# Optimization experiments

Hardware: AMD Instinct MI355X
Metric: run time of the kernel (lower is better)

The kernel has to match this reference:

```python
import jax, jax.numpy as jnp
import numpy as np

MD = 4  # max displacement -> 9x9 = 81 window, matches the +8 pad and 81 output channels


def setup_inputs() -> dict:
    key = jax.random.key(0)
    k1, k2 = jax.random.split(key)
    first = jax.random.normal(k1, (8, 256, 96, 128), dtype=jnp.float32)
    second = jax.random.normal(k2, (8, 256, 96, 128), dtype=jnp.float32)
    return {"first": first, "second": second}


def reference(first, second):
    # first, second: [B, C, H, W]
    B, C, H, W = first.shape
    # pad second spatially by MD on each side (the rbot1 [B, H+8, W+8, C] buffer)
    pad = jnp.pad(second, ((0, 0), (0, 0), (MD, MD), (MD, MD)))
    outs = []
    # channel ordering matches CUDA kernel: top_channel = (dy+4)*9 + (dx+4)
    for dy in range(2 * MD + 1):
        for dx in range(2 * MD + 1):
            shifted = jax.lax.dynamic_slice(pad, (0, 0, dy, dx), (B, C, H, W))
            outs.append(jnp.einsum('bchw,bchw->bhw', first, shifted))
    # kernel divides the per-pixel dot product by the channel count
    return jnp.stack(outs, axis=1) / C  # [B, 81, H, W]
```

## Files before the change

### kernel.cpp

```cpp
#include <hip/hip_runtime.h>

namespace {
constexpr int Bn = 8, Cn = 256, Hn = 96, Wn = 128;
constexpr int HWn = Hn * Wn;
constexpr int CHWn = Cn * HWn;
constexpr int ND = 9;
constexpr int TILESH = Hn / 4;
constexpr int NBLK = Bn * TILESH * ND;
constexpr int PERX = NBLK / 8;
}

__device__ __forceinline__ float dpp_shr1(float x) {
  return __int_as_float(__builtin_amdgcn_update_dpp(
      0, __float_as_int(x), 0x111 , 0xF, 0xF, true));
}
__device__ __forceinline__ float dpp_shl1(float x) {
  return __int_as_float(__builtin_amdgcn_update_dpp(
      0, __float_as_int(x), 0x101 , 0xF, 0xF, true));
}

struct Ch {
  float4 sa, sb, fa, fb;
};

__global__ __launch_bounds__(64, 2) void corr_kernel(
    const float* __restrict__ first, const float* __restrict__ second,
    float* __restrict__ out)
{
  const int lane = threadIdx.x;
  const int bid = blockIdx.x;
  const int logical = (bid & 7) * PERX + (bid >> 3);
  const int dy = logical % ND;
  const int t = logical / ND;
  const int b = t / TILESH;
  const int h0 = (t % TILESH) * 4;

  const int hs = lane >> 4;
  const int w0 = (lane & 15) << 3;

  const int gr = h0 + hs + dy - 4;
  const float m = (gr >= 0 && gr < Hn) ? 1.0f : 0.0f;
  const int cg = min(max(gr, 0), Hn - 1);

  const float* ssrc = second + b * CHWn + cg * Wn + w0;
  const float* fsrc = first + b * CHWn + (h0 + hs) * Wn + w0;

  float acc[ND][8];
#pragma unroll
  for (int dx = 0; dx < ND; ++dx)
#pragma unroll
    for (int p = 0; p < 8; ++p) acc[dx][p] = 0.f;

  auto LOADCH = [&](int coff) -> Ch {
    Ch r;
    r.sa = *(const float4*)(ssrc + coff);
    r.sb = *(const float4*)(ssrc + coff + 4);
    r.fa = *(const float4*)(fsrc + coff);
    r.fb = *(const float4*)(fsrc + coff + 4);
    return r;
  };

  auto COMP = [&](const Ch& ch) {
    const float sa0 = ch.sa.x * m, sa1 = ch.sa.y * m, sa2 = ch.sa.z * m, sa3 = ch.sa.w * m;
    const float sb0 = ch.sb.x * m, sb1 = ch.sb.y * m, sb2 = ch.sb.z * m, sb3 = ch.sb.w * m;
    const float s[16] = {
        dpp_shr1(sb0), dpp_shr1(sb1), dpp_shr1(sb2), dpp_shr1(sb3),
        sa0, sa1, sa2, sa3,
        sb0, sb1, sb2, sb3,
        dpp_shl1(sa0), dpp_shl1(sa1), dpp_shl1(sa2), dpp_shl1(sa3)};
    const float f[8] = {ch.fa.x, ch.fa.y, ch.fa.z, ch.fa.w,
                        ch.fb.x, ch.fb.y, ch.fb.z, ch.fb.w};
#pragma unroll
    for (int dx = 0; dx < ND; ++dx)
#pragma unroll
      for (int p = 0; p < 8; ++p)
        acc[dx][p] = fmaf(f[p], s[p + dx], acc[dx][p]);
  };

  Ch L0 = LOADCH(0);
  Ch L1 = LOADCH(HWn);
  int coff = 2 * HWn;
#pragma unroll 1
  for (int it = 0; it < (Cn - 2) / 2; ++it) {
    Ch N0 = LOADCH(coff);
    Ch N1 = LOADCH(coff + HWn);
    COMP(L0);
    COMP(L1);
    L0 = N0;
    L1 = N1;
    coff += 2 * HWn;
  }
  COMP(L0);
  COMP(L1);

  const float sc = 1.0f / Cn;
  float* obase = out + ((b * 81 + dy * ND) * Hn + (h0 + hs)) * Wn + w0;
#pragma unroll
  for (int dx = 0; dx < ND; ++dx) {
    float4 o0 = make_float4(acc[dx][0] * sc, acc[dx][1] * sc,
                            acc[dx][2] * sc, acc[dx][3] * sc);
    float4 o1 = make_float4(acc[dx][4] * sc, acc[dx][5] * sc,
                            acc[dx][6] * sc, acc[dx][7] * sc);
    *(float4*)(obase + dx * HWn) = o0;
    *(float4*)(obase + dx * HWn + 4) = o1;
  }
}

extern "C" void kernel_launch(void* const* d_in, const int* in_sizes, int n_in,
                              void* d_out, int out_size, void* d_ws, size_t ws_size,
                              hipStream_t stream) {
  const float* first = (const float*)d_in[0];
  const float* second = (const float*)d_in[1];
  float* out = (float*)d_out;
  corr_kernel<<<dim3(NBLK), dim3(64), 0, stream>>>(first, second, out);
}
```

Measured before the change: 98.27 us.

## Rewrite correlation as bf16 MFMA banded matmul with LDS double buffering

Replaces the scalar FP32 FMA correlation kernel with a block-tiled kernel. Each block stages first and padded second tiles in LDS as bf16, double-buffered across channel chunks of 32. It computes 32x32 banded dot-product tiles with MFMA 32x32x16 bf16 instructions, keeping only the 9-wide diagonal band per dy. Results are transposed through LDS so output stores are coalesced. This trades FP32 accuracy for bf16 inputs and wastes MFMA work on off-band entries, aiming to cut the FMA-bound compute cost.

```diff
diff --git a/kernel.cpp b/kernel.cpp
--- a/kernel.cpp
+++ b/kernel.cpp
@@ -1,108 +1,188 @@
 #include <hip/hip_runtime.h>
+
+typedef __attribute__((ext_vector_type(8))) short bf16x8;
+typedef __attribute__((ext_vector_type(16))) float f32x16;
 
 namespace {
 constexpr int Bn = 8, Cn = 256, Hn = 96, Wn = 128;
 constexpr int HWn = Hn * Wn;
-constexpr int CHWn = Cn * HWn;
-constexpr int ND = 9;
-constexpr int TILESH = Hn / 4;
-constexpr int NBLK = Bn * TILESH * ND;
-constexpr int PERX = NBLK / 8;
+constexpr int KC = 32;
+constexpr int SP = 40;
+constexpr int SW = 72;
+constexpr int SR = 6;
+constexpr int FW = 64;
+constexpr int SSZ = SR * SW * SP;
+constexpr int FSZ = (4 * FW + 8) * SP;
+constexpr int BUF = SSZ + FSZ;
+constexpr int NBLK = 8 * 24 * 2 * 3;
 }
 
-__device__ __forceinline__ float dpp_shr1(float x) {
-  return __int_as_float(__builtin_amdgcn_update_dpp(
-      0, __float_as_int(x), 0x111 , 0xF, 0xF, true));
-}
-__device__ __forceinline__ float dpp_shl1(float x) {
-  return __int_as_float(__builtin_amdgcn_update_dpp(
-      0, __float_as_int(x), 0x101 , 0xF, 0xF, true));
+__device__ __forceinline__ unsigned f2bfpk(float lo, float hi) {
+  unsigned a = __float_as_uint(lo), b = __float_as_uint(hi);
+  a = ((a + 0x7FFF + ((a >> 16) & 1)) >> 16) & 0xFFFF;
+  b = ((b + 0x7FFF + ((b >> 16) & 1)) >> 16) & 0xFFFF;
+  return (b << 16) | a;
 }
 
-struct Ch {
-  float4 sa, sb, fa, fb;
-};
-
-__global__ __launch_bounds__(64, 2) void corr_kernel(
+__global__ __launch_bounds__(768, 1) void corr_mfma(
     const float* __restrict__ first, const float* __restrict__ second,
     float* __restrict__ out)
 {
-  const int lane = threadIdx.x;
+  __shared__ __align__(16) unsigned short LB[2][BUF];
+
+  const int tid = threadIdx.x;
+  const int wv = tid >> 6;
+  const int lane = tid & 63;
+  const int ln31 = lane & 31;
+  const int half = lane >> 5;
+  const int li4 = lane >> 2;
+  const int lm4 = lane & 3;
+
   const int bid = blockIdx.x;
-  const int logical = (bid & 7) * PERX + (bid >> 3);
-  const int dy = logical % ND;
-  const int t = logical / ND;
-  const int b = t / TILESH;
-  const int h0 = (t % TILESH) * 4;
+  const int logical = (bid & 7) * (NBLK / 8) + (bid >> 3);
+  const int b = logical / 144;
+  int rest = logical % 144;
+  const int hq = rest / 6; rest %= 6;
+  const int wh = rest / 3;
+  const int dg = rest % 3;
+  const int h0 = hq * 4, wb = wh * 64;
+  const int rbase = h0 + dg * 3 - 4;
 
-  const int hs = lane >> 4;
-  const int w0 = (lane & 15) << 3;
+  const int hh = wv / 3;
+  const int tt = wv % 3;
+  const int toff = (tt == 0) ? 0 : (tt == 1) ? 24 : 40;
 
-  const int gr = h0 + hs + dy - 4;
-  const float m = (gr >= 0 && gr < Hn) ? 1.0f : 0.0f;
-  const int cg = min(max(gr, 0), Hn - 1);
+  f32x16 acc0 = {}, acc1 = {}, acc2 = {};
 
-  const float* ssrc = second + b * CHWn + cg * Wn + w0;
-  const float* fsrc = first + b * CHWn + (h0 + hs) * Wn + w0;
+  float sx[16][2];
 
-  float acc[ND][8];
+  auto LOADS = [&](int ck) {
 #pragma unroll
-  for (int dx = 0; dx < ND; ++dx)
+    for (int st = 0; st < 8; ++st) {
+      const int id = wv * 8 + st;
+      const int r = id >> 4, q = id & 15;
+      const int cl = ((q >> 2) << 3) + (lm4 << 1);
+      const int wi = ((q & 3) << 4) + li4;
+      const int rg = rbase + r, wg = wb - 4 + wi;
+      const int rgc = min(Hn - 1, max(0, rg));
+      const int wgc = min(Wn - 1, max(0, wg));
+      const bool v = (rg >= 0) & (rg < Hn) & (wg >= 0) & (wg < Wn);
+      const float* p = second + ((b * Cn + ck + cl) * Hn + rgc) * Wn + wgc;
+      sx[st][0] = v ? p[0] : 0.0f;
+      sx[st][1] = v ? p[HWn] : 0.0f;
+    }
 #pragma unroll
-    for (int p = 0; p < 8; ++p) acc[dx][p] = 0.f;
-
-  auto LOADCH = [&](int coff) -> Ch {
-    Ch r;
-    r.sa = *(const float4*)(ssrc + coff);
-    r.sb = *(const float4*)(ssrc + coff + 4);
-    r.fa = *(const float4*)(fsrc + coff);
-    r.fb = *(const float4*)(fsrc + coff + 4);
-    return r;
+    for (int pt = 0; pt < 2; ++pt) {
+      const int id = wv * 2 + pt;
+      const int r = id >> 2, cbi = id & 3;
+      const int cl = (cbi << 3) + (lm4 << 1);
+      const int wi = 64 + li4;
+      const int rg = rbase + r, wg = wb - 4 + wi;
+      const int rgc = min(Hn - 1, max(0, rg));
+      const int wgc = min(Wn - 1, max(0, wg));
+      const bool v = (lane < 32) & (rg >= 0) & (rg < Hn) & (wg >= 0) & (wg < Wn);
+      const float* p = second + ((b * Cn + ck + cl) * Hn + rgc) * Wn + wgc;
+      sx[8 + pt][0] = v ? p[0] : 0.0f;
+      sx[8 + pt][1] = v ? p[HWn] : 0.0f;
+    }
+#pragma unroll
+    for (int k = 0; k < 6; ++k) {
+      const int ft = wv + 12 * k;
+      if (ft < 64) {
+        const int hh2 = ft >> 4, q = ft & 15;
+        const int cl = ((q >> 2) << 3) + (lm4 << 1);
+        const int wl = ((q & 3) << 4) + li4;
+        const float* p = first + ((b * Cn + ck + cl) * Hn + h0 + hh2) * Wn + wb + wl;
+        sx[10 + k][0] = p[0];
+        sx[10 + k][1] = p[HWn];
+      }
+    }
   };
 
-  auto COMP = [&](const Ch& ch) {
-    const float sa0 = ch.sa.x * m, sa1 = ch.sa.y * m, sa2 = ch.sa.z * m, sa3 = ch.sa.w * m;
-    const float sb0 = ch.sb.x * m, sb1 = ch.sb.y * m, sb2 = ch.sb.z * m, sb3 = ch.sb.w * m;
-    const float s[16] = {
-        dpp_shr1(sb0), dpp_shr1(sb1), dpp_shr1(sb2), dpp_shr1(sb3),
-        sa0, sa1, sa2, sa3,
-        sb0, sb1, sb2, sb3,
-        dpp_shl1(sa0), dpp_shl1(sa1), dpp_shl1(sa2), dpp_shl1(sa3)};
-    const float f[8] = {ch.fa.x, ch.fa.y, ch.fa.z, ch.fa.w,
-                        ch.fb.x, ch.fb.y, ch.fb.z, ch.fb.w};
+  auto WRITES = [&](unsigned short* lb) {
 #pragma unroll
-    for (int dx = 0; dx < ND; ++dx)
+    for (int st = 0; st < 8; ++st) {
+      const int id = wv * 8 + st;
+      const int r = id >> 4, q = id & 15;
+      const int cl = ((q >> 2) << 3) + (lm4 << 1);
+      const int wi = ((q & 3) << 4) + li4;
+      *(unsigned*)&lb[(r * SW + wi) * SP + cl] = f2bfpk(sx[st][0], sx[st][1]);
+    }
 #pragma unroll
-      for (int p = 0; p < 8; ++p)
-        acc[dx][p] = fmaf(f[p], s[p + dx], acc[dx][p]);
+    for (int pt = 0; pt < 2; ++pt) {
+      const int id = wv * 2 + pt;
+      const int r = id >> 2, cbi = id & 3;
+      const int cl = (cbi << 3) + (lm4 << 1);
+      const int wi = 64 + li4;
+      if (lane < 32)
+        *(unsigned*)&lb[(r * SW + wi) * SP + cl] = f2bfpk(sx[8 + pt][0], sx[8 + pt][1]);
+    }
+#pragma unroll
+    for (int k = 0; k < 6; ++k) {
+      const int ft = wv + 12 * k;
+      if (ft < 64) {
+        const int hh2 = ft >> 4, q = ft & 15;
+        const int cl = ((q >> 2) << 3) + (lm4 << 1);
+        const int wl = ((q & 3) << 4) + li4;
+        *(unsigned*)&lb[SSZ + (hh2 * FW + wl) * SP + cl] = f2bfpk(sx[10 + k][0], sx[10 + k][1]);
+      }
+    }
   };
 
-  Ch L0 = LOADCH(0);
-  Ch L1 = LOADCH(HWn);
-  int coff = 2 * HWn;
-#pragma unroll 1
-  for (int it = 0; it < (Cn - 2) / 2; ++it) {
-    Ch N0 = LOADCH(coff);
-    Ch N1 = LOADCH(coff + HWn);
-    COMP(L0);
-    COMP(L1);
-    L0 = N0;
-    L1 = N1;
-    coff += 2 * HWn;
+  auto COMPUTE = [&](const unsigned short* sb) {
+    const unsigned short* fb = sb + SSZ;
+    const int abase = (hh * FW + toff + ln31) * SP + (half << 3);
+    bf16x8 a0 = *(const bf16x8*)(fb + abase);
+    bf16x8 a1 = *(const bf16x8*)(fb + abase + 16);
+    const int b0 = ((hh + 0) * SW + toff + ln31) * SP + (half << 3);
+    const int b1 = b0 + SW * SP;
+    const int b2 = b1 + SW * SP;
+    bf16x8 s00 = *(const bf16x8*)(sb + b0);
+    bf16x8 s01 = *(const bf16x8*)(sb + b0 + 16);
+    bf16x8 s10 = *(const bf16x8*)(sb + b1);
+    bf16x8 s11 = *(const bf16x8*)(sb + b1 + 16);
+    bf16x8 s20 = *(const bf16x8*)(sb + b2);
+    bf16x8 s21 = *(const bf16x8*)(sb + b2 + 16);
+    acc0 = __builtin_amdgcn_mfma_f32_32x32x16_bf16(a0, s00, acc0, 0, 0, 0);
+    acc0 = __builtin_amdgcn_mfma_f32_32x32x16_bf16(a1, s01, acc0, 0, 0, 0);
+    acc1 = __builtin_amdgcn_mfma_f32_32x32x16_bf16(a0, s10, acc1, 0, 0, 0);
+    acc1 = __builtin_amdgcn_mfma_f32_32x32x16_bf16(a1, s11, acc1, 0, 0, 0);
+    acc2 = __builtin_amdgcn_mfma_f32_32x32x16_bf16(a0, s20, acc2, 0, 0, 0);
+    acc2 = __builtin_amdgcn_mfma_f32_32x32x16_bf16(a1, s21, acc2, 0, 0, 0);
+  };
+
+  LOADS(0);
+  WRITES(&LB[0][0]);
+  __syncthreads();
+
+#pragma unroll 2
+  for (int k = 0; k < 8; ++k) {
+    if (k < 7) LOADS((k + 1) * KC);
+    COMPUTE(&LB[k & 1][0]);
+    if (k < 7) WRITES(&LB[(k + 1) & 1][0]);
+    __syncthreads();
   }
-  COMP(L0);
-  COMP(L1);
 
-  const float sc = 1.0f / Cn;
-  float* obase = out + ((b * 81 + dy * ND) * Hn + (h0 + hs)) * Wn + w0;
+  float* outl = (float*)&LB[0][0];
+  const float sc = 1.0f / 256.0f;
 #pragma unroll
-  for (int dx = 0; dx < ND; ++dx) {
-    float4 o0 = make_float4(acc[dx][0] * sc, acc[dx][1] * sc,
-                            acc[dx][2] * sc, acc[dx][3] * sc);
-    float4 o1 = make_float4(acc[dx][4] * sc, acc[dx][5] * sc,
-                            acc[dx][6] * sc, acc[dx][7] * sc);
-    *(float4*)(obase + dx * HWn) = o0;
-    *(float4*)(obase + dx * HWn + 4) = o1;
+  for (int dd = 0; dd < 3; ++dd) {
+    const f32x16& A = (dd == 0) ? acc0 : (dd == 1) ? acc1 : acc2;
+#pragma unroll
+    for (int q = 0; q < 16; ++q) {
+      const int m = (q & 3) + ((q >> 2) << 3) + (half << 2);
+      const int dxi = ln31 - m;
+      if (m < 24 && dxi >= 0 && dxi <= 8)
+        outl[(hh * FW + toff + m) * 29 + dd * 9 + dxi] = A[q] * sc;
+    }
+  }
+  __syncthreads();
+#pragma unroll
+  for (int k2 = 0; k2 < 9; ++k2) {
+    const int sp = wv + 12 * k2;
+    const int ch = sp % 27, hh2 = sp / 27;
+    out[((b * 81 + dg * 27 + ch) * Hn + h0 + hh2) * Wn + wb + lane] =
+        outl[(hh2 * FW + lane) * 29 + ch];
   }
 }
 
@@ -112,5 +192,5 @@
   const float* first = (const float*)d_in[0];
   const float* second = (const float*)d_in[1];
   float* out = (float*)d_out;
-  corr_kernel<<<dim3(NBLK), dim3(64), 0, stream>>>(first, second, out);
+  corr_mfma<<<dim3(NBLK), dim3(768), 0, stream>>>(first, second, out);
 }
```

Result: slower. 135.5 us (+37.9%).

## Fuse all dy into one block with LDS-tiled fp16 dot2 and channel-split atomics

Applied to the files above, without the earlier changes.

Replaces the per-dy 64-thread blocks with 576-thread blocks covering all nine dy offsets. Each block stages a halo tile of second and a tile of first into double-buffered LDS as packed fp16 channel pairs, and accumulates with v_dot2_f32_f16. The channel dimension is split in two across blocks, and partial sums are combined with atomic adds into a memset output. This removes the ninefold redundant global reads of first and second, but fp16 inputs lower precision and the atomics and memset add traffic.

```diff
diff --git a/kernel.cpp b/kernel.cpp
--- a/kernel.cpp
+++ b/kernel.cpp
@@ -1,108 +1,146 @@
 #include <hip/hip_runtime.h>
+
+typedef _Float16 half2v __attribute__((ext_vector_type(2)));
 
 namespace {
 constexpr int Bn = 8, Cn = 256, Hn = 96, Wn = 128;
 constexpr int HWn = Hn * Wn;
-constexpr int CHWn = Cn * HWn;
 constexpr int ND = 9;
-constexpr int TILESH = Hn / 4;
-constexpr int NBLK = Bn * TILESH * ND;
+constexpr int TH = 4, HQ = 24;
+constexpr int NBLK = Bn * HQ * 2 * 2;
 constexpr int PERX = NBLK / 8;
+constexpr int SP = 76;
+constexpr int FP = 68;
+constexpr int SSZ = 12 * SP;
+constexpr int STEP = SSZ + 4 * FP;
+constexpr int CHUNK = 2 * STEP;
+constexpr int NTASK = 560;
 }
 
-__device__ __forceinline__ float dpp_shr1(float x) {
-  return __int_as_float(__builtin_amdgcn_update_dpp(
-      0, __float_as_int(x), 0x111 , 0xF, 0xF, true));
-}
-__device__ __forceinline__ float dpp_shl1(float x) {
-  return __int_as_float(__builtin_amdgcn_update_dpp(
-      0, __float_as_int(x), 0x101 , 0xF, 0xF, true));
+__device__ __forceinline__ float dot2h(unsigned a, unsigned b, float c) {
+#if __has_builtin(__builtin_amdgcn_fdot2)
+  return __builtin_amdgcn_fdot2(__builtin_bit_cast(half2v, a),
+                                __builtin_bit_cast(half2v, b), c, false);
+#else
+  float d;
+  asm("v_dot2_f32_f16 %0, %1, %2, %3" : "=v"(d) : "v"(a), "v"(b), "v"(c));
+  return d;
+#endif
 }
 
-struct Ch {
-  float4 sa, sb, fa, fb;
-};
+__device__ __forceinline__ unsigned pkh(float lo, float hi) {
+  return __builtin_bit_cast(unsigned, __builtin_amdgcn_cvt_pkrtz(lo, hi));
+}
 
-__global__ __launch_bounds__(64, 2) void corr_kernel(
+__global__ __launch_bounds__(576, 6) void corr_fused(
     const float* __restrict__ first, const float* __restrict__ second,
     float* __restrict__ out)
 {
-  const int lane = threadIdx.x;
+  __shared__ __align__(16) unsigned LB[2][CHUNK];
+
+  const int tid = threadIdx.x;
+  const int dy = tid >> 6;
+  const int lane = tid & 63;
+  const int hs = lane >> 4;
+  const int w0 = (lane & 15) << 2;
+
   const int bid = blockIdx.x;
   const int logical = (bid & 7) * PERX + (bid >> 3);
-  const int dy = logical % ND;
-  const int t = logical / ND;
-  const int b = t / TILESH;
-  const int h0 = (t % TILESH) * 4;
+  const int b = logical / 96;
+  int rest = logical % 96;
+  const int ht = rest >> 2;
+  const int wh = (rest >> 1) & 1;
+  const int chalf = rest & 1;
+  const int h0 = ht * TH;
+  const int wb = wh * 64;
+  const int cbase = chalf * 128;
 
-  const int hs = lane >> 4;
-  const int w0 = (lane & 15) << 3;
+  const int stp = tid / 280;
+  const int t2 = tid % 280;
+  const bool isS = (t2 < 216);
+  const int srow = t2 / 18, sq = t2 % 18;
+  const int fr = (t2 - 216) >> 4, fq = (t2 - 216) & 15;
+  const int sgrow = h0 - 4 + srow;
+  const int sgcol = wb - 4 + 4 * sq;
+  const bool svalid = (sgrow >= 0) & (sgrow < Hn) & (sgcol >= 0) & (sgcol <= 124);
+  const int sgoff = ((b * Cn) * Hn + max(0, min(Hn - 1, sgrow))) * Wn +
+                    max(0, min(124, sgcol));
+  const int fgoff = ((b * Cn) * Hn + (h0 + fr)) * Wn + wb + 4 * fq;
+  const int ldst = stp * STEP + (isS ? (srow * SP + 4 * sq) : (SSZ + fr * FP + 4 * fq));
 
-  const int gr = h0 + hs + dy - 4;
-  const float m = (gr >= 0 && gr < Hn) ? 1.0f : 0.0f;
-  const int cg = min(max(gr, 0), Hn - 1);
-
-  const float* ssrc = second + b * CHWn + cg * Wn + w0;
-  const float* fsrc = first + b * CHWn + (h0 + hs) * Wn + w0;
-
-  float acc[ND][8];
+  float acc[ND][4];
 #pragma unroll
   for (int dx = 0; dx < ND; ++dx)
 #pragma unroll
-    for (int p = 0; p < 8; ++p) acc[dx][p] = 0.f;
+    for (int p = 0; p < 4; ++p) acc[dx][p] = 0.f;
 
-  auto LOADCH = [&](int coff) -> Ch {
-    Ch r;
-    r.sa = *(const float4*)(ssrc + coff);
-    r.sb = *(const float4*)(ssrc + coff + 4);
-    r.fa = *(const float4*)(fsrc + coff);
-    r.fb = *(const float4*)(fsrc + coff + 4);
-    return r;
+  float4 ga, gb;
+  auto LOADS = [&](int k) {
+    if (tid < NTASK) {
+      const int c0 = cbase + 4 * k + 2 * stp;
+      if (isS) {
+        ga = make_float4(0.f, 0.f, 0.f, 0.f);
+        gb = ga;
+        if (svalid) {
+          const float* p0 = second + c0 * HWn + sgoff;
+          ga = *(const float4*)(p0);
+          gb = *(const float4*)(p0 + HWn);
+        }
+      } else {
+        const float* p0 = first + c0 * HWn + fgoff;
+        ga = *(const float4*)(p0);
+        gb = *(const float4*)(p0 + HWn);
+      }
+    }
+  };
+  auto WRITES = [&](unsigned* lb) {
+    if (tid < NTASK) {
+      uint4 u;
+      u.x = pkh(ga.x, gb.x); u.y = pkh(ga.y, gb.y);
+      u.z = pkh(ga.z, gb.z); u.w = pkh(ga.w, gb.w);
+      *(uint4*)(lb + ldst) = u;
+    }
   };
 
-  auto COMP = [&](const Ch& ch) {
-    const float sa0 = ch.sa.x * m, sa1 = ch.sa.y * m, sa2 = ch.sa.z * m, sa3 = ch.sa.w * m;
-    const float sb0 = ch.sb.x * m, sb1 = ch.sb.y * m, sb2 = ch.sb.z * m, sb3 = ch.sb.w * m;
-    const float s[16] = {
-        dpp_shr1(sb0), dpp_shr1(sb1), dpp_shr1(sb2), dpp_shr1(sb3),
-        sa0, sa1, sa2, sa3,
-        sb0, sb1, sb2, sb3,
-        dpp_shl1(sa0), dpp_shl1(sa1), dpp_shl1(sa2), dpp_shl1(sa3)};
-    const float f[8] = {ch.fa.x, ch.fa.y, ch.fa.z, ch.fa.w,
-                        ch.fb.x, ch.fb.y, ch.fb.z, ch.fb.w};
+  auto COMPUTE = [&](const unsigned* lb) {
 #pragma unroll
-    for (int dx = 0; dx < ND; ++dx)
+    for (int s = 0; s < 2; ++s) {
+      const unsigned* base = lb + s * STEP;
+      const unsigned* sp = base + (hs + dy) * SP + w0;
+      uint4 s0 = *(const uint4*)(sp);
+      uint4 s1 = *(const uint4*)(sp + 4);
+      uint4 s2 = *(const uint4*)(sp + 8);
+      uint4 fx = *(const uint4*)(base + SSZ + hs * FP + w0);
+      const unsigned sw[12] = {s0.x, s0.y, s0.z, s0.w, s1.x, s1.y,
+                               s1.z, s1.w, s2.x, s2.y, s2.z, s2.w};
+      const unsigned fv[4] = {fx.x, fx.y, fx.z, fx.w};
 #pragma unroll
-      for (int p = 0; p < 8; ++p)
-        acc[dx][p] = fmaf(f[p], s[p + dx], acc[dx][p]);
+      for (int dx = 0; dx < ND; ++dx)
+#pragma unroll
+        for (int p = 0; p < 4; ++p)
+          acc[dx][p] = dot2h(fv[p], sw[p + dx], acc[dx][p]);
+    }
   };
 
-  Ch L0 = LOADCH(0);
-  Ch L1 = LOADCH(HWn);
-  int coff = 2 * HWn;
+  LOADS(0);
+  WRITES(&LB[0][0]);
+  __syncthreads();
 #pragma unroll 1
-  for (int it = 0; it < (Cn - 2) / 2; ++it) {
-    Ch N0 = LOADCH(coff);
-    Ch N1 = LOADCH(coff + HWn);
-    COMP(L0);
-    COMP(L1);
-    L0 = N0;
-    L1 = N1;
-    coff += 2 * HWn;
+  for (int k = 0; k < 32; ++k) {
+    if (k < 31) LOADS(k + 1);
+    COMPUTE(&LB[k & 1][0]);
+    if (k < 31) WRITES(&LB[(k + 1) & 1][0]);
+    __syncthreads();
   }
-  COMP(L0);
-  COMP(L1);
 
   const float sc = 1.0f / Cn;
-  float* obase = out + ((b * 81 + dy * ND) * Hn + (h0 + hs)) * Wn + w0;
+  float* ob = out + ((size_t)(b * 81 + dy * ND) * Hn + (h0 + hs)) * Wn + wb + w0;
 #pragma unroll
   for (int dx = 0; dx < ND; ++dx) {
-    float4 o0 = make_float4(acc[dx][0] * sc, acc[dx][1] * sc,
-                            acc[dx][2] * sc, acc[dx][3] * sc);
-    float4 o1 = make_float4(acc[dx][4] * sc, acc[dx][5] * sc,
-                            acc[dx][6] * sc, acc[dx][7] * sc);
-    *(float4*)(obase + dx * HWn) = o0;
-    *(float4*)(obase + dx * HWn + 4) = o1;
+    float* q = ob + (size_t)dx * HWn;
+#pragma unroll
+    for (int p = 0; p < 4; ++p)
+      unsafeAtomicAdd(q + p, acc[dx][p] * sc);
   }
 }
 
@@ -112,5 +150,6 @@
   const float* first = (const float*)d_in[0];
   const float* second = (const float*)d_in[1];
   float* out = (float*)d_out;
-  corr_kernel<<<dim3(NBLK), dim3(64), 0, stream>>>(first, second, out);
+  hipMemsetAsync(out, 0, (size_t)out_size * sizeof(float), stream);
+  corr_fused<<<dim3(NBLK), dim3(576), 0, stream>>>(first, second, out);
 }
```

Result: slower. 358.4 us (+264.7%).
